# Kernel tuning notes

Measured on AMD Instinct MI355X. Metric: run time of the kernel, lower is better.

Reference implementation:

```python
import jax, jax.numpy as jnp
import numpy as np

M, D, S, K, DIN = 512, 10, 16384, 1024, 784  # test points, classes, jacobian dim, n_eigh, input dim


def setup_inputs() -> dict:
    key = jax.random.key(0)
    k0, k1, k2, k3, k4 = jax.random.split(key, 5)
    X_test = jax.random.normal(k0, (M, DIN), dtype=jnp.float32)
    Jz = jax.random.normal(k1, (M, D, S), dtype=jnp.float32) * 0.02      # backend.jacobians(X_test)
    v = jax.random.normal(k2, (S, K), dtype=jnp.float32) * 0.02          # self.v from fit()
    A = jax.random.normal(k3, (K, K), dtype=jnp.float32) * 0.02
    G_inv = 0.5 * (A + A.T) + jnp.eye(K, dtype=jnp.float32)              # symmetric, like an inverse PSD matrix
    W_net = jax.random.normal(k4, (DIN, D), dtype=jnp.float32) * 0.02    # stand-in for self.net
    return {"X_test": X_test, "Jz": Jz, "v": v, "G_inv": G_inv, "W_net": W_net}


def reference(X_test, Jz, v, G_inv, W_net):
    # phi: (d, m, k) -- per-class ELLA features of each test point
    phi = jnp.einsum('mds,sk->dmk', Jz, v)
    # Full (class, class, n, m) covariance tensor, exactly as the torch module computes it
    K_test = jnp.einsum('ank,kg,bmg->abnm', phi, G_inv, phi)
    mean = X_test @ W_net                                # self.net(X_test)
    var = jnp.diagonal(K_test, axis1=-2, axis2=-1)       # (d, d, n) -- discards off-diagonal n,m
    return mean, jnp.transpose(var, (2, 0, 1))           # (n, d, d)
```

## Files before the change

kernel.cpp:

```cpp
#include <hip/hip_runtime.h>
#include <hip/hip_bf16.h>

#define M_PTS 512
#define D_CLS 10
#define S_DIM 16384
#define K_DIM 1024
#define DIN_  784
#define PHI_ELEMS (5120 * 1024)

typedef short  bf16x8  __attribute__((ext_vector_type(8)));
typedef float  f32x4   __attribute__((ext_vector_type(4)));
typedef ushort ushort8 __attribute__((ext_vector_type(8)));

__device__ __forceinline__ ushort f2bfu(float f) {
    __bf16 h = (__bf16)f;
    return __builtin_bit_cast(ushort, h);
}
__device__ __forceinline__ float bfu2f(ushort u) {
    uint x = (uint)u << 16;
    return __builtin_bit_cast(float, x);
}

__global__ __launch_bounds__(64) void mean_kernel(const float* __restrict__ X,
                                                  const float* __restrict__ W,
                                                  float* __restrict__ out) {
    int m = blockIdx.x;
    int lane = threadIdx.x;
    float acc[D_CLS];
#pragma unroll
    for (int d = 0; d < D_CLS; ++d) acc[d] = 0.f;
    for (int i = lane; i < DIN_; i += 64) {
        float x = X[(size_t)m * DIN_ + i];
#pragma unroll
        for (int d = 0; d < D_CLS; ++d) acc[d] += x * W[i * D_CLS + d];
    }
#pragma unroll
    for (int d = 0; d < D_CLS; ++d) {
        float v = acc[d];
        for (int off = 32; off > 0; off >>= 1) v += __shfl_down(v, off);
        if (lane == 0) out[(size_t)m * D_CLS + d] = v;
    }
}

__global__ __launch_bounds__(256) void cvt_a(const float* __restrict__ src,
                                             ushort* __restrict__ dst, int n8) {
    for (int i = blockIdx.x * 256 + threadIdx.x; i < n8; i += gridDim.x * 256) {
        float4 a = reinterpret_cast<const float4*>(src)[2 * i];
        float4 b = reinterpret_cast<const float4*>(src)[2 * i + 1];
        ushort8 o;
        o[0] = f2bfu(a.x); o[1] = f2bfu(a.y); o[2] = f2bfu(a.z); o[3] = f2bfu(a.w);
        o[4] = f2bfu(b.x); o[5] = f2bfu(b.y); o[6] = f2bfu(b.z); o[7] = f2bfu(b.w);
        reinterpret_cast<ushort8*>(dst)[i] = o;
    }
}

__global__ __launch_bounds__(256) void cvt_bt(const float* __restrict__ v,
                                              ushort* __restrict__ bt) {
    __shared__ float tile[64][65];
    const int kt = blockIdx.x;
    const int ct = blockIdx.y;
    const int t  = threadIdx.x;
    const int col4 = t & 15, row = t >> 4;
#pragma unroll
    for (int i = 0; i < 4; ++i) {
        int r = row + 16 * i;
        float4 v4 = *reinterpret_cast<const float4*>(
            v + (size_t)(kt * 64 + r) * K_DIM + ct * 64 + col4 * 4);
        tile[r][col4 * 4 + 0] = v4.x; tile[r][col4 * 4 + 1] = v4.y;
        tile[r][col4 * 4 + 2] = v4.z; tile[r][col4 * 4 + 3] = v4.w;
    }
    __syncthreads();
#pragma unroll
    for (int i = 0; i < 2; ++i) {
        int cid = i * 256 + t;
        int c = cid >> 3, kc = cid & 7;
        ushort8 o;
#pragma unroll
        for (int j = 0; j < 8; ++j) o[j] = f2bfu(tile[kc * 8 + j][c]);
        *reinterpret_cast<ushort8*>(bt + (size_t)(ct * 64 + c) * S_DIM +
                                    kt * 64 + kc * 8) = o;
    }
}

template <int KSP>
__global__ __launch_bounds__(256, 4) void gemm_cv(const float* __restrict__ A,
                                                  const ushort* __restrict__ BT,
                                                  ushort* __restrict__ Cout) {
    __shared__ ushort As[2][4096];
    __shared__ ushort Bs[2][4096];

    const int nwg = 320 * KSP;
    const int lid = blockIdx.x;
    const int swz = (lid & 7) * (nwg >> 3) + (lid >> 3);
    const int kp  = swz / 320;
    const int rem = swz - kp * 320;
    const int bm  = rem >> 3;
    const int bn  = rem & 7;
    const int KSTEPS = 512 / KSP;
    const int kbase  = kp * (S_DIM / KSP);

    const int t  = threadIdx.x;
    const int l  = t & 63;
    const int wm = (t >> 7) & 1;
    const int wn = (t >> 6) & 1;
    const int lr = l & 15;
    const int kq = l >> 4;

    const float*  Ablk = A  + (size_t)(bm * 128) * S_DIM + kbase;
    const ushort* Bblk = BT + (size_t)(bn * 128) * S_DIM + kbase;

    const int   ar   = t >> 2;
    const int   csrc = (t & 3) ^ ((t >> 3) & 3);
    const float* ag0 = Ablk + (size_t)ar * S_DIM + csrc * 8;
    const float* ag1 = ag0 + (size_t)64 * S_DIM;

    float4 rA[4], rB[4];

    f32x4 acc[4][4];
#pragma unroll
    for (int i = 0; i < 4; ++i)
#pragma unroll
        for (int j = 0; j < 4; ++j) acc[i][j] = (f32x4)0.f;

#define LOADA(P, S)                                                             \
    { P[0] = *reinterpret_cast<const float4*>(ag0 + (size_t)(S) * 32);          \
      P[1] = *reinterpret_cast<const float4*>(ag0 + (size_t)(S) * 32 + 4);      \
      P[2] = *reinterpret_cast<const float4*>(ag1 + (size_t)(S) * 32);          \
      P[3] = *reinterpret_cast<const float4*>(ag1 + (size_t)(S) * 32 + 4); }

#define WRITEA(BUF, P)                                                          \
    { ushort8 o0, o1;                                                           \
      o0[0] = f2bfu(P[0].x); o0[1] = f2bfu(P[0].y);                             \
      o0[2] = f2bfu(P[0].z); o0[3] = f2bfu(P[0].w);                             \
      o0[4] = f2bfu(P[1].x); o0[5] = f2bfu(P[1].y);                             \
      o0[6] = f2bfu(P[1].z); o0[7] = f2bfu(P[1].w);                             \
      o1[0] = f2bfu(P[2].x); o1[1] = f2bfu(P[2].y);                             \
      o1[2] = f2bfu(P[2].z); o1[3] = f2bfu(P[2].w);                             \
      o1[4] = f2bfu(P[3].x); o1[5] = f2bfu(P[3].y);                             \
      o1[6] = f2bfu(P[3].z); o1[7] = f2bfu(P[3].w);                             \
      *reinterpret_cast<ushort8*>(&As[BUF][t * 8])        = o0;                 \
      *reinterpret_cast<ushort8*>(&As[BUF][t * 8 + 2048]) = o1; }

#define STAGE_B(BUF, S)                                                         \
    { _Pragma("unroll") for (int i = 0; i < 2; ++i) {                           \
        const int cch = i * 256 + t;                                            \
        const int r = cch >> 2, sl = cch & 3;                                   \
        const ushort* gp = Bblk + (size_t)r * S_DIM + (S) * 32 +                \
                           ((sl ^ ((r >> 1) & 3)) << 3);                        \
        ushort* lp = &Bs[BUF][(i * 256 + (t & 192)) * 8];                       \
        __builtin_amdgcn_global_load_lds(                                       \
            (const __attribute__((address_space(1))) void*)gp,                  \
            (__attribute__((address_space(3))) void*)lp, 16, 0, 0);             \
      } }

#define COMPUTE(BUF)                                                            \
    { bf16x8 fa[4], fb[4];                                                      \
      _Pragma("unroll") for (int mi = 0; mi < 4; ++mi) {                        \
        const int r = wm * 64 + mi * 16 + lr;                                   \
        fa[mi] = *reinterpret_cast<const bf16x8*>(                              \
            &As[BUF][(r * 4 + (kq ^ ((r >> 1) & 3))) * 8]);                     \
      }                                                                         \
      _Pragma("unroll") for (int ni = 0; ni < 4; ++ni) {                        \
        const int c = wn * 64 + ni * 16 + lr;                                   \
        fb[ni] = *reinterpret_cast<const bf16x8*>(                              \
            &Bs[BUF][(c * 4 + (kq ^ ((c >> 1) & 3))) * 8]);                     \
      }                                                                         \
      _Pragma("unroll") for (int ni = 0; ni < 4; ++ni)                          \
        _Pragma("unroll") for (int mi = 0; mi < 4; ++mi)                        \
          acc[mi][ni] = __builtin_amdgcn_mfma_f32_16x16x32_bf16(                \
              fa[mi], fb[ni], acc[mi][ni], 0, 0, 0);                            \
    }

    LOADA(rA, 0)
    STAGE_B(0, 0)
    WRITEA(0, rA)
    LOADA(rB, 1)
    __syncthreads();

    const int NIT2 = KSTEPS / 2;
    for (int s2 = 0; s2 < NIT2; ++s2) {
        const int s = 2 * s2;
        if (s + 2 < KSTEPS) { LOADA(rA, s + 2) }
        STAGE_B(1, s + 1)
        WRITEA(1, rB)
        COMPUTE(0)
        __syncthreads();
        if (s + 3 < KSTEPS) { LOADA(rB, s + 3) }
        if (s + 2 < KSTEPS) {
            STAGE_B(0, s + 2)
            WRITEA(0, rA)
        }
        COMPUTE(1)
        __syncthreads();
    }

    ushort* C = Cout + (size_t)kp * PHI_ELEMS;
#pragma unroll
    for (int mi = 0; mi < 4; ++mi) {
        int orow = bm * 128 + wm * 64 + mi * 16 + kq * 4;
#pragma unroll
        for (int ni = 0; ni < 4; ++ni) {
            int ocol = bn * 128 + wn * 64 + ni * 16 + lr;
            ushort* cp = C + (size_t)orow * K_DIM + ocol;
#pragma unroll
            for (int rr = 0; rr < 4; ++rr)
                cp[(size_t)rr * K_DIM] = f2bfu(acc[mi][ni][rr]);
        }
    }
#undef LOADA
#undef WRITEA
#undef STAGE_B
#undef COMPUTE
}

template <int SD, int KSP>
__global__ __launch_bounds__(256, 3) void gemm_bb(const ushort* __restrict__ A,
                                                  const ushort* __restrict__ BT,
                                                  float* __restrict__ Cout) {
    __shared__ ushort As[3][4096];
    __shared__ ushort Bs[3][4096];

    const int nwg = 320 * KSP;
    const int lid = blockIdx.x;
    const int swz = (lid & 7) * (nwg >> 3) + (lid >> 3);
    const int kp  = swz / 320;
    const int rem = swz - kp * 320;
    const int bm  = rem >> 3;
    const int bn  = rem & 7;
    const int KSTEPS = SD / 32 / KSP;
    const int kbase  = kp * (SD / KSP);

    const int t  = threadIdx.x;
    const int l  = t & 63;
    const int wm = (t >> 7) & 1;
    const int wn = (t >> 6) & 1;
    const int lr = l & 15;
    const int kq = l >> 4;

    const ushort* Ablk = A  + (size_t)(bm * 128) * SD + kbase;
    const ushort* Bblk = BT + (size_t)(bn * 128) * SD + kbase;

    f32x4 acc[4][4];
#pragma unroll
    for (int i = 0; i < 4; ++i)
#pragma unroll
        for (int j = 0; j < 4; ++j) acc[i][j] = (f32x4)0.f;

#define GSTAGE(BUF, S, SRC, DST)                                                \
    { _Pragma("unroll") for (int i = 0; i < 2; ++i) {                           \
        const int cch = i * 256 + t;                                            \
        const int r = cch >> 2, sl = cch & 3;                                   \
        const ushort* gp = SRC + (size_t)r * SD + (S) * 32 +                    \
                           ((sl ^ ((r >> 1) & 3)) << 3);                        \
        ushort* lp = &DST[BUF][(i * 256 + (t & 192)) * 8];                      \
        __builtin_amdgcn_global_load_lds(                                       \
            (const __attribute__((address_space(1))) void*)gp,                  \
            (__attribute__((address_space(3))) void*)lp, 16, 0, 0);             \
      } }

#define GCOMPUTE(BUF)                                                           \
    { bf16x8 fa[4], fb[4];                                                      \
      _Pragma("unroll") for (int mi = 0; mi < 4; ++mi) {                        \
        const int r = wm * 64 + mi * 16 + lr;                                   \
        fa[mi] = *reinterpret_cast<const bf16x8*>(                              \
            &As[BUF][(r * 4 + (kq ^ ((r >> 1) & 3))) * 8]);                     \
      }                                                                         \
      _Pragma("unroll") for (int ni = 0; ni < 4; ++ni) {                        \
        const int c = wn * 64 + ni * 16 + lr;                                   \
        fb[ni] = *reinterpret_cast<const bf16x8*>(                              \
            &Bs[BUF][(c * 4 + (kq ^ ((c >> 1) & 3))) * 8]);                     \
      }                                                                         \
      _Pragma("unroll") for (int ni = 0; ni < 4; ++ni)                          \
        _Pragma("unroll") for (int mi = 0; mi < 4; ++mi)                        \
          acc[mi][ni] = __builtin_amdgcn_mfma_f32_16x16x32_bf16(                \
              fa[mi], fb[ni], acc[mi][ni], 0, 0, 0);                            \
    }

    GSTAGE(0, 0, Ablk, As)
    GSTAGE(0, 0, Bblk, Bs)
    GSTAGE(1, 1, Ablk, As)
    GSTAGE(1, 1, Bblk, Bs)
    asm volatile("s_waitcnt vmcnt(4)" ::: "memory");
    __builtin_amdgcn_s_barrier();
    __builtin_amdgcn_sched_barrier(0);

    for (int s = 0; s < KSTEPS - 2; ++s) {
        const int sb = (s + 2) % 3, cb = s % 3;
        GSTAGE(sb, s + 2, Ablk, As)
        GSTAGE(sb, s + 2, Bblk, Bs)
        __builtin_amdgcn_s_setprio(1);
        GCOMPUTE(cb)
        __builtin_amdgcn_s_setprio(0);
        __builtin_amdgcn_sched_barrier(0);
        asm volatile("s_waitcnt vmcnt(4)" ::: "memory");
        __builtin_amdgcn_s_barrier();
        __builtin_amdgcn_sched_barrier(0);
    }
    {
        __builtin_amdgcn_s_setprio(1);
        GCOMPUTE((KSTEPS - 2) % 3)
        __builtin_amdgcn_s_setprio(0);
        __builtin_amdgcn_sched_barrier(0);
        asm volatile("s_waitcnt vmcnt(0)" ::: "memory");
        __builtin_amdgcn_s_barrier();
        __builtin_amdgcn_sched_barrier(0);
        GCOMPUTE((KSTEPS - 1) % 3)
    }

    float* C = Cout + (size_t)kp * PHI_ELEMS;
#pragma unroll
    for (int mi = 0; mi < 4; ++mi) {
        int orow = bm * 128 + wm * 64 + mi * 16 + kq * 4;
#pragma unroll
        for (int ni = 0; ni < 4; ++ni) {
            int ocol = bn * 128 + wn * 64 + ni * 16 + lr;
            float* cp = C + (size_t)orow * K_DIM + ocol;
#pragma unroll
            for (int rr = 0; rr < 4; ++rr) cp[(size_t)rr * K_DIM] = acc[mi][ni][rr];
        }
    }
#undef GSTAGE
#undef GCOMPUTE
}

template <int KSP>
__global__ __launch_bounds__(256) void phi_reduceN(const ushort* __restrict__ slabs,
                                                   ushort* __restrict__ phib) {
    const int n8 = PHI_ELEMS / 8;
    for (int i = blockIdx.x * 256 + threadIdx.x; i < n8; i += gridDim.x * 256) {
        float s[8] = {0.f, 0.f, 0.f, 0.f, 0.f, 0.f, 0.f, 0.f};
#pragma unroll
        for (int p = 0; p < KSP; ++p) {
            ushort8 u = reinterpret_cast<const ushort8*>(
                slabs + (size_t)p * PHI_ELEMS)[i];
#pragma unroll
            for (int j = 0; j < 8; ++j) s[j] += bfu2f(u[j]);
        }
        ushort8 o;
#pragma unroll
        for (int j = 0; j < 8; ++j) o[j] = f2bfu(s[j]);
        reinterpret_cast<ushort8*>(phib)[i] = o;
    }
}

__global__ __launch_bounds__(256) void var_contract_b(const float* __restrict__ T,
                                                      const ushort* __restrict__ P,
                                                      float* __restrict__ out) {
    __shared__ float red[4][56];
    const int n = blockIdx.x, t = threadIdx.x, lane = t & 63, wid = t >> 6;
    const float*  Tn = T + (size_t)n * D_CLS * K_DIM;
    const ushort* Pn = P + (size_t)n * D_CLS * K_DIM;
    float Ta[D_CLS][4], Pb[D_CLS][4];
#pragma unroll
    for (int a = 0; a < D_CLS; ++a)
#pragma unroll
        for (int j = 0; j < 4; ++j) {
            Ta[a][j] = Tn[a * K_DIM + t + 256 * j];
            Pb[a][j] = bfu2f(Pn[a * K_DIM + t + 256 * j]);
        }
    int p = 0;
#pragma unroll
    for (int a = 0; a < D_CLS; ++a)
#pragma unroll
        for (int b = 0; b <= a; ++b, ++p) {
            float s = Ta[a][0] * Pb[b][0] + Ta[a][1] * Pb[b][1]
                    + Ta[a][2] * Pb[b][2] + Ta[a][3] * Pb[b][3];
#pragma unroll
            for (int off = 32; off > 0; off >>= 1) s += __shfl_down(s, off);
            if (lane == 0) red[wid][p] = s;
        }
    __syncthreads();
    if (t < 55) {
        int a = 0;
        while ((a + 1) * (a + 2) / 2 <= t) ++a;
        int b = t - a * (a + 1) / 2;
        float s = red[0][t] + red[1][t] + red[2][t] + red[3][t];
        float* vout = out + M_PTS * D_CLS + (size_t)n * D_CLS * D_CLS;
        vout[a * D_CLS + b] = s;
        vout[b * D_CLS + a] = s;
    }
}

extern "C" void kernel_launch(void* const* d_in, const int* in_sizes, int n_in,
                              void* d_out, int out_size, void* d_ws, size_t ws_size,
                              hipStream_t stream) {
    const float* X  = (const float*)d_in[0];
    const float* Jz = (const float*)d_in[1];
    const float* v  = (const float*)d_in[2];
    const float* G  = (const float*)d_in[3];
    const float* W  = (const float*)d_in[4];
    float* out = (float*)d_out;
    float* ws  = (float*)d_ws;

    const size_t PHB  = (size_t)PHI_ELEMS * 2;
    const size_t BT_B = (size_t)K_DIM * S_DIM * 2;
    const size_t G_B  = (size_t)K_DIM * K_DIM * 2;
    const size_t NEED4 = 4 * PHB + BT_B + G_B;
    const size_t NEED1 = PHB + BT_B + G_B + (size_t)PHI_ELEMS * 4;
    (void)NEED1;

    hipLaunchKernelGGL(mean_kernel, dim3(M_PTS), dim3(64), 0, stream, X, W, out);

    const int KSP = (ws_size >= NEED4) ? 4 : 1;
    ushort* slabs = (ushort*)ws;
    ushort* vTb   = slabs + (size_t)KSP * PHI_ELEMS;
    ushort* Gb    = vTb + (size_t)K_DIM * S_DIM;
    ushort* phib  = slabs;
    float*  T     = (KSP == 4) ? (float*)(slabs + (size_t)2 * PHI_ELEMS)
                               : (float*)(Gb + (size_t)K_DIM * K_DIM);

    hipLaunchKernelGGL(cvt_bt, dim3(256, 16), dim3(256), 0, stream, v, vTb);
    hipLaunchKernelGGL(cvt_a, dim3(256), dim3(256), 0, stream,
                       G, Gb, K_DIM * K_DIM / 8);
    if (KSP == 4) {
        hipLaunchKernelGGL(gemm_cv<4>, dim3(1280), dim3(256), 0, stream,
                           Jz, vTb, slabs);
        hipLaunchKernelGGL(phi_reduceN<4>, dim3(1024), dim3(256), 0, stream,
                           slabs, phib);
    } else {
        hipLaunchKernelGGL(gemm_cv<1>, dim3(320), dim3(256), 0, stream,
                           Jz, vTb, slabs);
    }
    hipLaunchKernelGGL((gemm_bb<K_DIM, 1>), dim3(320), dim3(256), 0, stream,
                       phib, Gb, T);
    hipLaunchKernelGGL(var_contract_b, dim3(M_PTS), dim3(256), 0, stream,
                       T, phib, out);
}
```

Measured before the change: 424.0 us.

## Triple-buffer B tiles and replace syncthreads with explicit waitcnt-based pipeline

The Jz×v GEMM now keeps three LDS buffers for the B operand and issues each B tile two steps ahead. Full __syncthreads are replaced by manual vmcnt/lgkmcnt waits, raw s_barrier and sched_barrier fences, and setprio raises wave priority around the MFMA blocks. The goal is more overlap of global-to-LDS traffic with MFMA compute and fewer barrier stalls. In exchange, LDS use per block grows and the launch bound drops from 4 to 3 blocks per CU. The hand-written vmcnt counts must also match the number of loads in flight, or results will be wrong.

```diff
diff --git a/kernel.cpp b/kernel.cpp
--- a/kernel.cpp
+++ b/kernel.cpp
@@ -83,11 +83,11 @@
 }
 
 template <int KSP>
-__global__ __launch_bounds__(256, 4) void gemm_cv(const float* __restrict__ A,
-                                                  const ushort* __restrict__ BT,
-                                                  ushort* __restrict__ Cout) {
+__global__ __launch_bounds__(256, 3) void gemm_cvp(const float* __restrict__ A,
+                                                   const ushort* __restrict__ BT,
+                                                   ushort* __restrict__ Cout) {
     __shared__ ushort As[2][4096];
-    __shared__ ushort Bs[2][4096];
+    __shared__ ushort Bs[3][4096];
 
     const int nwg = 320 * KSP;
     const int lid = blockIdx.x;
@@ -153,17 +153,17 @@
             (__attribute__((address_space(3))) void*)lp, 16, 0, 0);             \
       } }
 
-#define COMPUTE(BUF)                                                            \
+#define COMPUTE(AB, BB)                                                         \
     { bf16x8 fa[4], fb[4];                                                      \
       _Pragma("unroll") for (int mi = 0; mi < 4; ++mi) {                        \
         const int r = wm * 64 + mi * 16 + lr;                                   \
         fa[mi] = *reinterpret_cast<const bf16x8*>(                              \
-            &As[BUF][(r * 4 + (kq ^ ((r >> 1) & 3))) * 8]);                     \
+            &As[AB][(r * 4 + (kq ^ ((r >> 1) & 3))) * 8]);                      \
       }                                                                         \
       _Pragma("unroll") for (int ni = 0; ni < 4; ++ni) {                        \
         const int c = wn * 64 + ni * 16 + lr;                                   \
         fb[ni] = *reinterpret_cast<const bf16x8*>(                              \
-            &Bs[BUF][(c * 4 + (kq ^ ((c >> 1) & 3))) * 8]);                     \
+            &Bs[BB][(c * 4 + (kq ^ ((c >> 1) & 3))) * 8]);                      \
       }                                                                         \
       _Pragma("unroll") for (int ni = 0; ni < 4; ++ni)                          \
         _Pragma("unroll") for (int mi = 0; mi < 4; ++mi)                        \
@@ -171,27 +171,47 @@
               fa[mi], fb[ni], acc[mi][ni], 0, 0, 0);                            \
     }
 
+    STAGE_B(0, 0)
     LOADA(rA, 0)
-    STAGE_B(0, 0)
+    STAGE_B(1, 1)
+    LOADA(rB, 1)
+    asm volatile("s_waitcnt vmcnt(6)" ::: "memory");
     WRITEA(0, rA)
-    LOADA(rB, 1)
-    __syncthreads();
+    asm volatile("s_waitcnt lgkmcnt(0)" ::: "memory");
+    __builtin_amdgcn_s_barrier();
+    __builtin_amdgcn_sched_barrier(0);
 
     const int NIT2 = KSTEPS / 2;
     for (int s2 = 0; s2 < NIT2; ++s2) {
         const int s = 2 * s2;
-        if (s + 2 < KSTEPS) { LOADA(rA, s + 2) }
-        STAGE_B(1, s + 1)
+        if (s + 2 < KSTEPS) {
+            LOADA(rA, s + 2)
+            STAGE_B((s + 2) % 3, s + 2)
+        }
+        __builtin_amdgcn_s_setprio(1);
+        COMPUTE(0, s % 3)
+        __builtin_amdgcn_s_setprio(0);
+        __builtin_amdgcn_sched_barrier(0);
+        if (s + 2 < KSTEPS) { asm volatile("s_waitcnt vmcnt(6)" ::: "memory"); }
+        else                { asm volatile("s_waitcnt vmcnt(0)" ::: "memory"); }
         WRITEA(1, rB)
-        COMPUTE(0)
-        __syncthreads();
-        if (s + 3 < KSTEPS) { LOADA(rB, s + 3) }
-        if (s + 2 < KSTEPS) {
-            STAGE_B(0, s + 2)
-            WRITEA(0, rA)
-        }
-        COMPUTE(1)
-        __syncthreads();
+        asm volatile("s_waitcnt lgkmcnt(0)" ::: "memory");
+        __builtin_amdgcn_s_barrier();
+        __builtin_amdgcn_sched_barrier(0);
+        if (s + 3 < KSTEPS) {
+            LOADA(rB, s + 3)
+            STAGE_B((s + 3) % 3, s + 3)
+        }
+        __builtin_amdgcn_s_setprio(1);
+        COMPUTE(1, (s + 1) % 3)
+        __builtin_amdgcn_s_setprio(0);
+        __builtin_amdgcn_sched_barrier(0);
+        if (s + 3 < KSTEPS) { asm volatile("s_waitcnt vmcnt(6)" ::: "memory"); }
+        else                { asm volatile("s_waitcnt vmcnt(0)" ::: "memory"); }
+        if (s + 2 < KSTEPS) { WRITEA(0, rA) }
+        asm volatile("s_waitcnt lgkmcnt(0)" ::: "memory");
+        __builtin_amdgcn_s_barrier();
+        __builtin_amdgcn_sched_barrier(0);
     }
 
     ushort* C = Cout + (size_t)kp * PHI_ELEMS;
@@ -413,12 +433,12 @@
     hipLaunchKernelGGL(cvt_a, dim3(256), dim3(256), 0, stream,
                        G, Gb, K_DIM * K_DIM / 8);
     if (KSP == 4) {
-        hipLaunchKernelGGL(gemm_cv<4>, dim3(1280), dim3(256), 0, stream,
+        hipLaunchKernelGGL(gemm_cvp<4>, dim3(1280), dim3(256), 0, stream,
                            Jz, vTb, slabs);
         hipLaunchKernelGGL(phi_reduceN<4>, dim3(1024), dim3(256), 0, stream,
                            slabs, phib);
     } else {
-        hipLaunchKernelGGL(gemm_cv<1>, dim3(320), dim3(256), 0, stream,
+        hipLaunchKernelGGL(gemm_cvp<1>, dim3(320), dim3(256), 0, stream,
                            Jz, vTb, slabs);
     }
     hipLaunchKernelGGL((gemm_bb<K_DIM, 1>), dim3(320), dim3(256), 0, stream,
```

Result: slower. 438.4 us (+3.4%).
